# Kernel optimization log

Measured on AMD Instinct MI355X. Metric: run time of the kernel, lower is better.

The kernel has to match this reference:

```python
import jax, jax.numpy as jnp
import numpy as np

N_NODES = 100000
N_EDGES = 3200000
D_IN = 256
D_OUT = 256


def setup_inputs() -> dict:
    key = jax.random.key(0)
    k1, k2, k3, k4, k5 = jax.random.split(key, 5)
    x = jax.random.normal(k1, (N_NODES, D_IN), dtype=jnp.float32)
    weight = jax.random.normal(k2, (D_IN, D_OUT), dtype=jnp.float32)
    edge_rows = jax.random.randint(k3, (N_EDGES,), 0, N_NODES, dtype=jnp.int32)
    edge_cols = jax.random.randint(k4, (N_EDGES,), 0, N_NODES, dtype=jnp.int32)
    edge_vals = jax.random.uniform(k5, (N_EDGES,), dtype=jnp.float32)
    return {"x": x, "weight": weight, "edge_rows": edge_rows,
            "edge_cols": edge_cols, "edge_vals": edge_vals}


def reference(x, weight, edge_rows, edge_cols, edge_vals):
    # GraphConvolution forward (eval mode, dense features, no bias):
    #   xw  = x @ W                      [N, D_OUT]
    #   out = relu(A_sparse @ xw)        A given as COO edge list
    xw = x @ weight  # [N, D_OUT]
    msgs = edge_vals[:, None] * xw[edge_cols]  # gather source features, scale
    agg = jax.ops.segment_sum(msgs, edge_rows, num_segments=N_NODES)
    return jax.nn.relu(agg)
```

## Files before the change

kernel.cpp:

```cpp
#include <hip/hip_runtime.h>
#include <hip/hip_bf16.h>

#define N_NODES 100000
#define N_EDGES 3200000
#define D 256

#define RSH3 6
#define RPB3 64
#define NB3 ((N_NODES + RPB3 - 1) / RPB3)
#define FILL_CH 14336
#define NBLK_F ((N_EDGES + FILL_CH - 1) / FILL_CH)
#define RCAP 12
#define SCAP 3072
#define OCAP 64

typedef __attribute__((ext_vector_type(8))) short short8;
typedef __attribute__((ext_vector_type(4))) float floatx4;

__device__ __forceinline__ unsigned short f32_to_bf16_rne(float f) {
    unsigned int u = __float_as_uint(f);
    u += 0x7FFFu + ((u >> 16) & 1u);
    return (unsigned short)(u >> 16);
}
__device__ __forceinline__ float bf16_bits_to_f32(unsigned short b) {
    return __uint_as_float(((unsigned int)b) << 16);
}
__device__ __forceinline__ float blo(unsigned int x) { return __uint_as_float(x << 16); }
__device__ __forceinline__ float bhi(unsigned int x) { return __uint_as_float(x & 0xFFFF0000u); }

__global__ __launch_bounds__(256) void convert_w_k(const float* __restrict__ w,
                                                   unsigned short* __restrict__ wsw) {
    int t = blockIdx.x * 256 + threadIdx.x;
    int j     = t & 7;
    int lane  = (t >> 3) & 63;
    int kstep = (t >> 9) & 7;
    int ntile = t >> 12;
    int k = kstep * 32 + (lane >> 4) * 8 + j;
    int n = ntile * 16 + (lane & 15);
    wsw[t] = f32_to_bf16_rne(w[k * D + n]);
}

__global__ __launch_bounds__(512) void gemm_xw_k(const float* __restrict__ x,
                                                 const unsigned short* __restrict__ wsw,
                                                 unsigned short* __restrict__ xwb) {
    __shared__ uint4 wlds[8192];
    const int tid = threadIdx.x;
#pragma unroll
    for (int i = 0; i < 16; ++i) {
        int idx = i * 512 + tid;
        wlds[idx] = ((const uint4*)wsw)[idx];
    }
    __syncthreads();

    const int lane = tid & 63;
    const int wave = tid >> 6;
    const int q    = lane >> 4;
    const int ml   = lane & 15;
    const long rowBase = (long)blockIdx.x * 128;
    long arow = rowBase + wave * 16 + ml;
    if (arow >= N_NODES) arow = 0;
    const float* xr = x + arow * (long)D;

    floatx4 acc[16];
#pragma unroll
    for (int i = 0; i < 16; ++i) acc[i] = (floatx4){0.f, 0.f, 0.f, 0.f};

    const short8* wfrag = (const short8*)wlds;

#pragma unroll
    for (int ks = 0; ks < 8; ++ks) {
        const float4 a0 = *(const float4*)(xr + ks * 32 + q * 8);
        const float4 a1 = *(const float4*)(xr + ks * 32 + q * 8 + 4);
        short8 af;
        af[0] = (short)f32_to_bf16_rne(a0.x);
        af[1] = (short)f32_to_bf16_rne(a0.y);
        af[2] = (short)f32_to_bf16_rne(a0.z);
        af[3] = (short)f32_to_bf16_rne(a0.w);
        af[4] = (short)f32_to_bf16_rne(a1.x);
        af[5] = (short)f32_to_bf16_rne(a1.y);
        af[6] = (short)f32_to_bf16_rne(a1.z);
        af[7] = (short)f32_to_bf16_rne(a1.w);
#pragma unroll
        for (int nt = 0; nt < 16; ++nt) {
            acc[nt] = __builtin_amdgcn_mfma_f32_16x16x32_bf16(
                af, wfrag[(nt * 8 + ks) * 64 + lane], acc[nt], 0, 0, 0);
        }
    }

    __syncthreads();
    unsigned short* lds16 = (unsigned short*)wlds;
#pragma unroll
    for (int nt = 0; nt < 16; ++nt) {
#pragma unroll
        for (int r = 0; r < 4; ++r) {
            int rowL = wave * 16 + q * 4 + r;
            int chunk = (nt * 2 + (ml >> 3)) ^ (rowL & 7);
            lds16[rowL * 256 + chunk * 8 + (ml & 7)] = f32_to_bf16_rne(acc[nt][r]);
        }
    }
    __syncthreads();
    {
        int rowL = tid >> 2;
        long gRow = rowBase + rowL;
        if (gRow < N_NODES) {
            const uint4* src = (const uint4*)(lds16 + rowL * 256);
            uint4* dst = (uint4*)(xwb + gRow * (long)D);
#pragma unroll
            for (int c8 = 0; c8 < 8; ++c8) {
                int chunk = (tid & 3) * 8 + c8;
                dst[chunk] = src[chunk ^ (rowL & 7)];
            }
        }
    }
}

__global__ __launch_bounds__(256) void hist2_k(const int* __restrict__ erow,
                                               int* __restrict__ C) {
    __shared__ int h[NB3];
    const int tid = threadIdx.x;
    for (int i = tid; i < NB3; i += 256) h[i] = 0;
    __syncthreads();
    const int s = blockIdx.x * FILL_CH;
    const int e = min(s + FILL_CH, N_EDGES);
    for (int i = s + tid; i < e; i += 256) atomicAdd(&h[erow[i] >> RSH3], 1);
    __syncthreads();
    for (int b = tid; b < NB3; b += 256) C[b * NBLK_F + blockIdx.x] = h[b];
}

__global__ __launch_bounds__(256) void colprefix_k(int* __restrict__ C,
                                                   int* __restrict__ tot) {
    const int wave_id = blockIdx.x * 4 + (threadIdx.x >> 6);
    const int lane = threadIdx.x & 63;
    if (wave_id >= NB3) return;
    int* row = C + wave_id * NBLK_F;
    int run = 0;
#pragma unroll
    for (int ch = 0; ch < NBLK_F; ch += 64) {
        int idx = ch + lane;
        int v = (idx < NBLK_F) ? row[idx] : 0;
        int x = v;
#pragma unroll
        for (int d = 1; d < 64; d <<= 1) {
            int u = __shfl_up(x, d);
            if (lane >= d) x += u;
        }
        int excl = x - v;
        if (idx < NBLK_F) row[idx] = run + excl;
        run += __shfl(x, 63);
    }
    if (lane == 0) tot[wave_id] = run;
}

__global__ __launch_bounds__(1024) void totscan_k(const int* __restrict__ tot,
                                                  int* __restrict__ bbase) {
    __shared__ int wsum[16];
    const int t = threadIdx.x;
    const int lane = t & 63;
    const int wv = t >> 6;
    const int b0 = 2 * t, b1 = 2 * t + 1;
    int v0 = (b0 < NB3) ? tot[b0] : 0;
    int v1 = (b1 < NB3) ? tot[b1] : 0;
    int sv = v0 + v1;
    int x = sv;
#pragma unroll
    for (int d = 1; d < 64; d <<= 1) {
        int u = __shfl_up(x, d);
        if (lane >= d) x += u;
    }
    if (lane == 63) wsum[wv] = x;
    __syncthreads();
    if (wv == 0) {
        int y = (lane < 16) ? wsum[lane] : 0;
#pragma unroll
        for (int d = 1; d < 16; d <<= 1) {
            int u = __shfl_up(y, d);
            if (lane >= d) y += u;
        }
        if (lane < 16) wsum[lane] = y;
    }
    __syncthreads();
    int excl = x - sv + ((wv > 0) ? wsum[wv - 1] : 0);
    if (b0 < NB3) bbase[b0] = excl;
    if (b1 < NB3) bbase[b1] = excl + v0;
    if (b0 == NB3 - 1) bbase[NB3] = excl + v0;
    if (b1 == NB3 - 1) bbase[NB3] = excl + v0 + v1;
}

__global__ __launch_bounds__(512) void binfill3_k(const int* __restrict__ erow,
                                                  const int* __restrict__ ecol,
                                                  const float* __restrict__ eval,
                                                  const int* __restrict__ C,
                                                  const int* __restrict__ bbase,
                                                  unsigned long long* __restrict__ recs) {
    __shared__ unsigned long long lrec[FILL_CH];
    __shared__ int h[NB3];
    __shared__ int cur[NB3];
    __shared__ int gb[NB3];
    __shared__ int wsum[8];
    const int tid = threadIdx.x;
    const int blk = blockIdx.x;
    const int s = blk * FILL_CH;
    const int e = min(s + FILL_CH, N_EDGES);

    for (int i = tid; i < NB3; i += 512) h[i] = 0;
    __syncthreads();

    for (int i = s + tid; i < e; i += 512) atomicAdd(&h[erow[i] >> RSH3], 1);
    __syncthreads();

    {
        const int b0 = 4 * tid;
        int v0 = (b0     < NB3) ? h[b0]     : 0;
        int v1 = (b0 + 1 < NB3) ? h[b0 + 1] : 0;
        int v2 = (b0 + 2 < NB3) ? h[b0 + 2] : 0;
        int v3 = (b0 + 3 < NB3) ? h[b0 + 3] : 0;
        int s4 = v0 + v1 + v2 + v3;
        const int lane = tid & 63;
        const int wv = tid >> 6;
        int x = s4;
#pragma unroll
        for (int d = 1; d < 64; d <<= 1) {
            int u = __shfl_up(x, d);
            if (lane >= d) x += u;
        }
        if (lane == 63) wsum[wv] = x;
        __syncthreads();
        if (wv == 0) {
            int y = (lane < 8) ? wsum[lane] : 0;
#pragma unroll
            for (int d = 1; d < 8; d <<= 1) {
                int u = __shfl_up(y, d);
                if (lane >= d) y += u;
            }
            if (lane < 8) wsum[lane] = y;
        }
        __syncthreads();
        int excl = x - s4 + ((wv > 0) ? wsum[wv - 1] : 0);
        if (b0     < NB3) cur[b0]     = excl;
        if (b0 + 1 < NB3) cur[b0 + 1] = excl + v0;
        if (b0 + 2 < NB3) cur[b0 + 2] = excl + v0 + v1;
        if (b0 + 3 < NB3) cur[b0 + 3] = excl + v0 + v1 + v2;
    }
    for (int b = tid; b < NB3; b += 512) gb[b] = bbase[b] + C[b * NBLK_F + blk];
    __syncthreads();

    for (int i = s + tid; i < e; i += 512) {
        int r = erow[i];
        int b = r >> RSH3;
        unsigned long long rec =
            ((unsigned long long)(r & (RPB3 - 1)) << 33) |
            ((unsigned long long)f32_to_bf16_rne(eval[i]) << 17) |
            (unsigned int)ecol[i];
        int pos = atomicAdd(&cur[b], 1);
        lrec[pos] = rec;
    }
    __syncthreads();

    const int lane = tid & 63;
    const int wv = tid >> 6;
    for (int b = wv; b < NB3; b += 8) {
        int len = h[b];
        int start = cur[b] - len;
        int gdst = gb[b];
        for (int o = lane; o < len; o += 64) recs[gdst + o] = lrec[start + o];
    }
}

__global__ __launch_bounds__(256) void baggr_k(const unsigned short* __restrict__ xwb,
                                               const int* __restrict__ bbase,
                                               const unsigned long long* __restrict__ recs,
                                               float* __restrict__ out) {
    __shared__ unsigned int   cols[SCAP];
    __shared__ unsigned short vals[SCAP];
    __shared__ unsigned long long ovfl[OCAP];
    __shared__ int hist[RPB3];
    __shared__ int cur[RPB3];
    __shared__ int novf;
    const int t = threadIdx.x;
    const int b = blockIdx.x;
    const int base = bbase[b];
    const int bend = bbase[b + 1];

    if (t < RPB3) hist[t] = 0;
    if (t == 0) novf = 0;
    __syncthreads();

    unsigned long long myrec[RCAP];
#pragma unroll
    for (int k = 0; k < RCAP; ++k) {
        int idx = base + k * 256 + t;
        if (idx < bend) myrec[k] = recs[idx];
    }
#pragma unroll
    for (int k = 0; k < RCAP; ++k) {
        int idx = base + k * 256 + t;
        if (idx < bend) atomicAdd(&hist[(int)((myrec[k] >> 33) & 63u)], 1);
    }
    for (int i = base + RCAP * 256 + t; i < bend; i += 256)
        atomicAdd(&hist[(int)((recs[i] >> 33) & 63u)], 1);
    __syncthreads();

    if (t < 64) {
        int v = hist[t];
        int x = v;
#pragma unroll
        for (int d = 1; d < 64; d <<= 1) {
            int u = __shfl_up(x, d);
            if (t >= d) x += u;
        }
        cur[t] = x - v;
    }
    __syncthreads();

#pragma unroll
    for (int k = 0; k < RCAP; ++k) {
        int idx = base + k * 256 + t;
        if (idx < bend) {
            unsigned long long rec = myrec[k];
            int rl = (int)((rec >> 33) & 63u);
            int pos = atomicAdd(&cur[rl], 1);
            if (pos < SCAP) {
                cols[pos] = (unsigned int)(rec & 0x1FFFFu);
                vals[pos] = (unsigned short)((rec >> 17) & 0xFFFFu);
            } else {
                int o = atomicAdd(&novf, 1);
                if (o < OCAP) ovfl[o] = rec;
            }
        }
    }
    for (int i = base + RCAP * 256 + t; i < bend; i += 256) {
        unsigned long long rec = recs[i];
        int rl = (int)((rec >> 33) & 63u);
        int pos = atomicAdd(&cur[rl], 1);
        if (pos < SCAP) {
            cols[pos] = (unsigned int)(rec & 0x1FFFFu);
            vals[pos] = (unsigned short)((rec >> 17) & 0xFFFFu);
        } else {
            int o = atomicAdd(&novf, 1);
            if (o < OCAP) ovfl[o] = rec;
        }
    }
    __syncthreads();

    const int wave = t >> 6;
    const int lane = t & 63;
    const int half = lane >> 5;
    const int hl   = lane & 31;
    const int nov  = min(novf, OCAP);

#pragma unroll 1
    for (int rr = 0; rr < 16; ++rr) {
        const int rl = wave * 16 + rr;
        const int r = (b << RSH3) + rl;
        if (r >= N_NODES) break;
        const int e_ = cur[rl];
        const int s_ = e_ - hist[rl];
        const int e = min(e_, SCAP);
        const int s = min(s_, SCAP);

        float acc[8];
#pragma unroll
        for (int k = 0; k < 8; ++k) acc[k] = 0.f;

#pragma unroll 1
        for (int jb = s; jb < e; jb += 64) {
            const int cnt = min(64, e - jb);
            const int pairs = (cnt + 1) >> 1;
            const int hp = cnt >> 1;
            int tt = 0;

#define FMA8(qv, bv)                                                           \
            acc[0] += bv * blo(qv.x); acc[1] += bv * bhi(qv.x);                \
            acc[2] += bv * blo(qv.y); acc[3] += bv * bhi(qv.y);                \
            acc[4] += bv * blo(qv.z); acc[5] += bv * bhi(qv.z);                \
            acc[6] += bv * blo(qv.w); acc[7] += bv * bhi(qv.w);
#define SLOTL(ss, qv, bv)                                                      \
            {                                                                  \
                int src = jb + 2 * (tt + (ss)) + half;                         \
                unsigned int bc = cols[src];                                   \
                bv = bf16_bits_to_f32(vals[src]);                              \
                qv = ((const uint4*)(xwb + (size_t)bc * D))[hl];               \
            }

#pragma unroll 1
            for (; tt + 8 <= hp; tt += 8) {
                uint4 q0, q1, q2, q3, q4, q5, q6, q7;
                float b0, b1, b2, b3, b4, b5, b6, b7;
                SLOTL(0, q0, b0) SLOTL(1, q1, b1) SLOTL(2, q2, b2) SLOTL(3, q3, b3)
                SLOTL(4, q4, b4) SLOTL(5, q5, b5) SLOTL(6, q6, b6) SLOTL(7, q7, b7)
                FMA8(q0, b0) FMA8(q1, b1) FMA8(q2, b2) FMA8(q3, b3)
                FMA8(q4, b4) FMA8(q5, b5) FMA8(q6, b6) FMA8(q7, b7)
            }
            if (tt + 4 <= hp) {
                uint4 q0, q1, q2, q3;
                float b0, b1, b2, b3;
                SLOTL(0, q0, b0) SLOTL(1, q1, b1) SLOTL(2, q2, b2) SLOTL(3, q3, b3)
                FMA8(q0, b0) FMA8(q1, b1) FMA8(q2, b2) FMA8(q3, b3)
                tt += 4;
            }
#undef SLOTL
#pragma unroll 1
            for (; tt < pairs; ++tt) {
                int src = jb + 2 * tt + half;
                int srcc = min(src, e - 1);
                unsigned int bc = cols[srcc];
                float vv = bf16_bits_to_f32(vals[srcc]);
                float bv = (src < e) ? vv : 0.f;
                uint4 q = ((const uint4*)(xwb + (size_t)bc * D))[hl];
                FMA8(q, bv)
            }
        }

#pragma unroll 1
        for (int k = 0; k < nov; ++k) {
            unsigned long long rec = ovfl[k];
            if ((int)((rec >> 33) & 63u) == rl) {
                unsigned int bc = (unsigned int)(rec & 0x1FFFFu);
                float vv = bf16_bits_to_f32((unsigned short)((rec >> 17) & 0xFFFFu));
                float bv = (half == 0) ? vv : 0.f;
                uint4 q = ((const uint4*)(xwb + (size_t)bc * D))[hl];
                FMA8(q, bv)
            }
        }
#undef FMA8

#pragma unroll
        for (int k = 0; k < 8; ++k) acc[k] += __shfl_xor(acc[k], 32);

        const int sl = lane >> 1;
        const int par = lane & 1;
        float4 o;
        {
            float a0 = __shfl(acc[0], sl), c0 = __shfl(acc[4], sl);
            float a1 = __shfl(acc[1], sl), c1 = __shfl(acc[5], sl);
            float a2 = __shfl(acc[2], sl), c2 = __shfl(acc[6], sl);
            float a3 = __shfl(acc[3], sl), c3 = __shfl(acc[7], sl);
            o.x = par ? c0 : a0;
            o.y = par ? c1 : a1;
            o.z = par ? c2 : a2;
            o.w = par ? c3 : a3;
        }
        o.x = fmaxf(o.x, 0.f);
        o.y = fmaxf(o.y, 0.f);
        o.z = fmaxf(o.z, 0.f);
        o.w = fmaxf(o.w, 0.f);
        ((float4*)(out + (size_t)r * D))[lane] = o;
    }
}

extern "C" void kernel_launch(void* const* d_in, const int* in_sizes, int n_in,
                              void* d_out, int out_size, void* d_ws, size_t ws_size,
                              hipStream_t stream) {
    const float* x    = (const float*)d_in[0];
    const float* w    = (const float*)d_in[1];
    const int*   erow = (const int*)d_in[2];
    const int*   ecol = (const int*)d_in[3];
    const float* eval = (const float*)d_in[4];
    float* out = (float*)d_out;

    char* p = (char*)d_ws;
    auto align = [](size_t v) { return (v + 255) & ~(size_t)255; };

    unsigned short* xwb = (unsigned short*)p;
    p += align((size_t)N_NODES * D * sizeof(unsigned short));
    unsigned short* wsw = (unsigned short*)p;
    p += align((size_t)D * D * sizeof(unsigned short));
    int* C     = (int*)p;  p += align((size_t)NB3 * NBLK_F * sizeof(int));
    int* tot   = (int*)p;  p += align((size_t)NB3 * sizeof(int));
    int* bbase = (int*)p;  p += align((size_t)(NB3 + 1) * sizeof(int));
    unsigned long long* recs = (unsigned long long*)p;
    p += align((size_t)N_EDGES * sizeof(unsigned long long));

    convert_w_k<<<(D * D) / 256, 256, 0, stream>>>(w, wsw);
    gemm_xw_k<<<(N_NODES + 127) / 128, 512, 0, stream>>>(x, wsw, xwb);
    hist2_k<<<NBLK_F, 256, 0, stream>>>(erow, C);
    colprefix_k<<<(NB3 + 3) / 4, 256, 0, stream>>>(C, tot);
    totscan_k<<<1, 1024, 0, stream>>>(tot, bbase);
    binfill3_k<<<NBLK_F, 512, 0, stream>>>(erow, ecol, eval, C, bbase, recs);
    baggr_k<<<NB3, 256, 0, stream>>>(xwb, bbase, recs, out);
}
```

Measured before the change: 554.6 us.

## Drop global edge binning prefix passes; aggregate via per-chunk local offsets

Removes the separate histogram, column-prefix and total-scan kernels. Each fill block now sorts its own edge chunk into bins locally and writes per-chunk bin offsets, and the aggregation block rebuilds its segment list with a shared-memory scan plus a binary search per record. This cuts three launches and the global scatter to bin positions, but adds per-block offset gathers and scattered record reads in aggregation. The GEMM epilogue also drops the LDS-staged coalesced store in favour of direct strided bf16 stores, and the fill chunk size shrinks.

Result: faster. 491.6 us (-11.4%).

```diff
diff --git a/kernel.cpp b/kernel.cpp
--- a/kernel.cpp
+++ b/kernel.cpp
@@ -8,8 +8,9 @@
 #define RSH3 6
 #define RPB3 64
 #define NB3 ((N_NODES + RPB3 - 1) / RPB3)
-#define FILL_CH 14336
+#define FILL_CH 8192
 #define NBLK_F ((N_EDGES + FILL_CH - 1) / FILL_CH)
+#define CLOC_W (NB3 + 1)
 #define RCAP 12
 #define SCAP 3072
 #define OCAP 64
@@ -56,8 +57,8 @@
     const int wave = tid >> 6;
     const int q    = lane >> 4;
     const int ml   = lane & 15;
-    const long rowBase = (long)blockIdx.x * 128;
-    long arow = rowBase + wave * 16 + ml;
+    const long rowBase = (long)blockIdx.x * 128 + wave * 16;
+    long arow = rowBase + ml;
     if (arow >= N_NODES) arow = 0;
     const float* xr = x + arow * (long)D;
 
@@ -87,120 +88,31 @@
         }
     }
 
-    __syncthreads();
-    unsigned short* lds16 = (unsigned short*)wlds;
 #pragma unroll
     for (int nt = 0; nt < 16; ++nt) {
 #pragma unroll
         for (int r = 0; r < 4; ++r) {
-            int rowL = wave * 16 + q * 4 + r;
-            int chunk = (nt * 2 + (ml >> 3)) ^ (rowL & 7);
-            lds16[rowL * 256 + chunk * 8 + (ml & 7)] = f32_to_bf16_rne(acc[nt][r]);
-        }
-    }
-    __syncthreads();
-    {
-        int rowL = tid >> 2;
-        long gRow = rowBase + rowL;
-        if (gRow < N_NODES) {
-            const uint4* src = (const uint4*)(lds16 + rowL * 256);
-            uint4* dst = (uint4*)(xwb + gRow * (long)D);
-#pragma unroll
-            for (int c8 = 0; c8 < 8; ++c8) {
-                int chunk = (tid & 3) * 8 + c8;
-                dst[chunk] = src[chunk ^ (rowL & 7)];
-            }
-        }
-    }
-}
-
-__global__ __launch_bounds__(256) void hist2_k(const int* __restrict__ erow,
-                                               int* __restrict__ C) {
-    __shared__ int h[NB3];
-    const int tid = threadIdx.x;
-    for (int i = tid; i < NB3; i += 256) h[i] = 0;
-    __syncthreads();
-    const int s = blockIdx.x * FILL_CH;
-    const int e = min(s + FILL_CH, N_EDGES);
-    for (int i = s + tid; i < e; i += 256) atomicAdd(&h[erow[i] >> RSH3], 1);
-    __syncthreads();
-    for (int b = tid; b < NB3; b += 256) C[b * NBLK_F + blockIdx.x] = h[b];
-}
-
-__global__ __launch_bounds__(256) void colprefix_k(int* __restrict__ C,
-                                                   int* __restrict__ tot) {
-    const int wave_id = blockIdx.x * 4 + (threadIdx.x >> 6);
-    const int lane = threadIdx.x & 63;
-    if (wave_id >= NB3) return;
-    int* row = C + wave_id * NBLK_F;
-    int run = 0;
-#pragma unroll
-    for (int ch = 0; ch < NBLK_F; ch += 64) {
-        int idx = ch + lane;
-        int v = (idx < NBLK_F) ? row[idx] : 0;
-        int x = v;
-#pragma unroll
-        for (int d = 1; d < 64; d <<= 1) {
-            int u = __shfl_up(x, d);
-            if (lane >= d) x += u;
-        }
-        int excl = x - v;
-        if (idx < NBLK_F) row[idx] = run + excl;
-        run += __shfl(x, 63);
-    }
-    if (lane == 0) tot[wave_id] = run;
-}
-
-__global__ __launch_bounds__(1024) void totscan_k(const int* __restrict__ tot,
-                                                  int* __restrict__ bbase) {
-    __shared__ int wsum[16];
-    const int t = threadIdx.x;
-    const int lane = t & 63;
-    const int wv = t >> 6;
-    const int b0 = 2 * t, b1 = 2 * t + 1;
-    int v0 = (b0 < NB3) ? tot[b0] : 0;
-    int v1 = (b1 < NB3) ? tot[b1] : 0;
-    int sv = v0 + v1;
-    int x = sv;
-#pragma unroll
-    for (int d = 1; d < 64; d <<= 1) {
-        int u = __shfl_up(x, d);
-        if (lane >= d) x += u;
-    }
-    if (lane == 63) wsum[wv] = x;
-    __syncthreads();
-    if (wv == 0) {
-        int y = (lane < 16) ? wsum[lane] : 0;
-#pragma unroll
-        for (int d = 1; d < 16; d <<= 1) {
-            int u = __shfl_up(y, d);
-            if (lane >= d) y += u;
-        }
-        if (lane < 16) wsum[lane] = y;
-    }
-    __syncthreads();
-    int excl = x - sv + ((wv > 0) ? wsum[wv - 1] : 0);
-    if (b0 < NB3) bbase[b0] = excl;
-    if (b1 < NB3) bbase[b1] = excl + v0;
-    if (b0 == NB3 - 1) bbase[NB3] = excl + v0;
-    if (b1 == NB3 - 1) bbase[NB3] = excl + v0 + v1;
-}
-
-__global__ __launch_bounds__(512) void binfill3_k(const int* __restrict__ erow,
-                                                  const int* __restrict__ ecol,
-                                                  const float* __restrict__ eval,
-                                                  const int* __restrict__ C,
-                                                  const int* __restrict__ bbase,
-                                                  unsigned long long* __restrict__ recs) {
+            long orow = rowBase + q * 4 + r;
+            if (orow < N_NODES)
+                xwb[orow * (long)D + nt * 16 + ml] = f32_to_bf16_rne(acc[nt][r]);
+        }
+    }
+}
+
+__global__ __launch_bounds__(512) void bfill_k(const int* __restrict__ erow,
+                                               const int* __restrict__ ecol,
+                                               const float* __restrict__ eval,
+                                               int* __restrict__ Cloc,
+                                               unsigned long long* __restrict__ recs) {
     __shared__ unsigned long long lrec[FILL_CH];
     __shared__ int h[NB3];
     __shared__ int cur[NB3];
-    __shared__ int gb[NB3];
     __shared__ int wsum[8];
     const int tid = threadIdx.x;
     const int blk = blockIdx.x;
     const int s = blk * FILL_CH;
     const int e = min(s + FILL_CH, N_EDGES);
+    const int n = e - s;
 
     for (int i = tid; i < NB3; i += 512) h[i] = 0;
     __syncthreads();
@@ -236,12 +148,13 @@
         }
         __syncthreads();
         int excl = x - s4 + ((wv > 0) ? wsum[wv - 1] : 0);
-        if (b0     < NB3) cur[b0]     = excl;
-        if (b0 + 1 < NB3) cur[b0 + 1] = excl + v0;
-        if (b0 + 2 < NB3) cur[b0 + 2] = excl + v0 + v1;
-        if (b0 + 3 < NB3) cur[b0 + 3] = excl + v0 + v1 + v2;
-    }
-    for (int b = tid; b < NB3; b += 512) gb[b] = bbase[b] + C[b * NBLK_F + blk];
+        int* crow = Cloc + (size_t)blk * CLOC_W;
+        if (b0     < NB3) { cur[b0]     = excl;                crow[b0]     = excl; }
+        if (b0 + 1 < NB3) { cur[b0 + 1] = excl + v0;           crow[b0 + 1] = excl + v0; }
+        if (b0 + 2 < NB3) { cur[b0 + 2] = excl + v0 + v1;      crow[b0 + 2] = excl + v0 + v1; }
+        if (b0 + 3 < NB3) { cur[b0 + 3] = excl + v0 + v1 + v2; crow[b0 + 3] = excl + v0 + v1 + v2; }
+        if (tid == 0) crow[NB3] = n;
+    }
     __syncthreads();
 
     for (int i = s + tid; i < e; i += 512) {
@@ -256,48 +169,97 @@
     }
     __syncthreads();
 
-    const int lane = tid & 63;
-    const int wv = tid >> 6;
-    for (int b = wv; b < NB3; b += 8) {
-        int len = h[b];
-        int start = cur[b] - len;
-        int gdst = gb[b];
-        for (int o = lane; o < len; o += 64) recs[gdst + o] = lrec[start + o];
-    }
+    unsigned long long* grow = recs + (size_t)blk * FILL_CH;
+    for (int i = tid; i < n; i += 512) grow[i] = lrec[i];
+}
+
+__device__ __forceinline__ unsigned long long fetch_rec(
+    const unsigned long long* __restrict__ recs,
+    const unsigned short* __restrict__ S,
+    const unsigned short* __restrict__ P, int i) {
+    int lo = 0, hi = NBLK_F;
+#pragma unroll
+    for (int it = 0; it < 9; ++it) {
+        int mid = (lo + hi) >> 1;
+        if ((int)P[mid] <= i) lo = mid; else hi = mid;
+    }
+    return recs[(size_t)lo * FILL_CH + (int)S[lo] + (i - (int)P[lo])];
 }
 
 __global__ __launch_bounds__(256) void baggr_k(const unsigned short* __restrict__ xwb,
-                                               const int* __restrict__ bbase,
+                                               const int* __restrict__ Cloc,
                                                const unsigned long long* __restrict__ recs,
                                                float* __restrict__ out) {
     __shared__ unsigned int   cols[SCAP];
     __shared__ unsigned short vals[SCAP];
     __shared__ unsigned long long ovfl[OCAP];
+    __shared__ unsigned short S[NBLK_F];
+    __shared__ unsigned short L[NBLK_F];
+    __shared__ unsigned short P[NBLK_F + 1];
     __shared__ int hist[RPB3];
     __shared__ int cur[RPB3];
+    __shared__ int wsum4[4];
     __shared__ int novf;
     const int t = threadIdx.x;
     const int b = blockIdx.x;
-    const int base = bbase[b];
-    const int bend = bbase[b + 1];
 
     if (t < RPB3) hist[t] = 0;
     if (t == 0) novf = 0;
-    __syncthreads();
+    for (int j = t; j < NBLK_F; j += 256) {
+        const int* crow = Cloc + (size_t)j * CLOC_W + b;
+        int a = crow[0], c = crow[1];
+        S[j] = (unsigned short)a;
+        L[j] = (unsigned short)(c - a);
+    }
+    __syncthreads();
+
+    {
+        const int j0 = 2 * t, j1 = 2 * t + 1;
+        int v0 = (j0 < NBLK_F) ? (int)L[j0] : 0;
+        int v1 = (j1 < NBLK_F) ? (int)L[j1] : 0;
+        int sv = v0 + v1;
+        const int lane = t & 63;
+        const int wv = t >> 6;
+        int x = sv;
+#pragma unroll
+        for (int d = 1; d < 64; d <<= 1) {
+            int u = __shfl_up(x, d);
+            if (lane >= d) x += u;
+        }
+        if (lane == 63) wsum4[wv] = x;
+        __syncthreads();
+        if (wv == 0) {
+            int y = (lane < 4) ? wsum4[lane] : 0;
+#pragma unroll
+            for (int d = 1; d < 4; d <<= 1) {
+                int u = __shfl_up(y, d);
+                if (lane >= d) y += u;
+            }
+            if (lane < 4) wsum4[lane] = y;
+        }
+        __syncthreads();
+        int excl = x - sv + ((wv > 0) ? wsum4[wv - 1] : 0);
+        if (j0 < NBLK_F) P[j0] = (unsigned short)excl;
+        if (j1 < NBLK_F) P[j1] = (unsigned short)(excl + v0);
+        if (j0 == NBLK_F - 1) P[NBLK_F] = (unsigned short)(excl + v0);
+        if (j1 == NBLK_F - 1) P[NBLK_F] = (unsigned short)(excl + v0 + v1);
+    }
+    __syncthreads();
+    const int nfull = (int)P[NBLK_F];
 
     unsigned long long myrec[RCAP];
 #pragma unroll
     for (int k = 0; k < RCAP; ++k) {
-        int idx = base + k * 256 + t;
-        if (idx < bend) myrec[k] = recs[idx];
+        int i = k * 256 + t;
+        if (i < nfull) myrec[k] = fetch_rec(recs, S, P, i);
     }
 #pragma unroll
     for (int k = 0; k < RCAP; ++k) {
-        int idx = base + k * 256 + t;
-        if (idx < bend) atomicAdd(&hist[(int)((myrec[k] >> 33) & 63u)], 1);
-    }
-    for (int i = base + RCAP * 256 + t; i < bend; i += 256)
-        atomicAdd(&hist[(int)((recs[i] >> 33) & 63u)], 1);
+        int i = k * 256 + t;
+        if (i < nfull) atomicAdd(&hist[(int)((myrec[k] >> 33) & 63u)], 1);
+    }
+    for (int i = SCAP + t; i < nfull; i += 256)
+        atomicAdd(&hist[(int)((fetch_rec(recs, S, P, i) >> 33) & 63u)], 1);
     __syncthreads();
 
     if (t < 64) {
@@ -314,8 +276,8 @@
 
 #pragma unroll
     for (int k = 0; k < RCAP; ++k) {
-        int idx = base + k * 256 + t;
-        if (idx < bend) {
+        int i = k * 256 + t;
+        if (i < nfull) {
             unsigned long long rec = myrec[k];
             int rl = (int)((rec >> 33) & 63u);
             int pos = atomicAdd(&cur[rl], 1);
@@ -328,8 +290,8 @@
             }
         }
     }
-    for (int i = base + RCAP * 256 + t; i < bend; i += 256) {
-        unsigned long long rec = recs[i];
+    for (int i = SCAP + t; i < nfull; i += 256) {
+        unsigned long long rec = fetch_rec(recs, S, P, i);
         int rl = (int)((rec >> 33) & 63u);
         int pos = atomicAdd(&cur[rl], 1);
         if (pos < SCAP) {
@@ -465,17 +427,13 @@
     p += align((size_t)N_NODES * D * sizeof(unsigned short));
     unsigned short* wsw = (unsigned short*)p;
     p += align((size_t)D * D * sizeof(unsigned short));
-    int* C     = (int*)p;  p += align((size_t)NB3 * NBLK_F * sizeof(int));
-    int* tot   = (int*)p;  p += align((size_t)NB3 * sizeof(int));
-    int* bbase = (int*)p;  p += align((size_t)(NB3 + 1) * sizeof(int));
+    int* Cloc = (int*)p;
+    p += align((size_t)NBLK_F * CLOC_W * sizeof(int));
     unsigned long long* recs = (unsigned long long*)p;
-    p += align((size_t)N_EDGES * sizeof(unsigned long long));
+    p += align((size_t)NBLK_F * FILL_CH * sizeof(unsigned long long));
 
     convert_w_k<<<(D * D) / 256, 256, 0, stream>>>(w, wsw);
     gemm_xw_k<<<(N_NODES + 127) / 128, 512, 0, stream>>>(x, wsw, xwb);
-    hist2_k<<<NBLK_F, 256, 0, stream>>>(erow, C);
-    colprefix_k<<<(NB3 + 3) / 4, 256, 0, stream>>>(C, tot);
-    totscan_k<<<1, 1024, 0, stream>>>(tot, bbase);
-    binfill3_k<<<NBLK_F, 512, 0, stream>>>(erow, ecol, eval, C, bbase, recs);
-    baggr_k<<<NB3, 256, 0, stream>>>(xwb, bbase, recs, out);
-}
+    bfill_k<<<NBLK_F, 512, 0, stream>>>(erow, ecol, eval, Cloc, recs);
+    baggr_k<<<NB3, 256, 0, stream>>>(xwb, Cloc, recs, out);
+}
```
